# Kernel optimization log

Measured on AMD Instinct MI355X. Metric: run time of the kernel, lower is better.

The kernel has to match this reference:

```python
import jax, jax.numpy as jnp
import numpy as np

B = 1024; NOBJ = 8; NPAIRS = 28; NREL = 8; NNEG = NPAIRS - NREL
NFS = 2048; EFS = 1024; H1 = 128; H2 = 512

# upper-triangle pair ordering, identical to label_locating_matrix construction
_tri = np.array([(i, j) for i in range(NOBJ) for j in range(i + 1, NOBJ)], dtype=np.int64)
PAIR_I = jnp.asarray(_tri[:, 0])
PAIR_J = jnp.asarray(_tri[:, 1])
_llm = np.full((NOBJ, NOBJ), -1, dtype=np.int64)
for _p, (_i, _j) in enumerate(_tri):
    _llm[_i, _j] = _p
    _llm[_j, _i] = _p
LLM = jnp.asarray(_llm)


def setup_inputs() -> dict:
    key = jax.random.key(0)
    ks = jax.random.split(key, 12)
    # 8 distinct (i<j) object pairs per batch element
    rng = np.random.default_rng(0)
    locs = np.argsort(rng.random((B, NPAIRS)), axis=1)[:, :NREL]  # [B, 8] distinct pair slots
    object_pairs = jnp.asarray(_tri[locs])  # [B, 8, 2]
    s = 0.02
    return {
        "node_features": jax.random.normal(ks[0], (B, NOBJ, NFS), jnp.float32),
        "interaction_feature": jax.random.normal(ks[1], (B, NOBJ, NOBJ, EFS), jnp.float32),
        "object_pairs": object_pairs,
        "W_ind1": jax.random.normal(ks[2], (NFS + EFS, H1), jnp.float32) * s,
        "b_ind1": jnp.zeros((H1,), jnp.float32),
        "W_ind2": jax.random.normal(ks[3], (H1, 1), jnp.float32) * s,
        "b_ind2": jnp.zeros((1,), jnp.float32),
        "W_rel": jax.random.normal(ks[4], (NFS + EFS + H1, H2), jnp.float32) * s,
        "b_rel": jnp.zeros((H2,), jnp.float32),
        "W_cr": jax.random.normal(ks[5], (H2, 3), jnp.float32) * s,
        "b_cr": jnp.zeros((3,), jnp.float32),
        "W_lr": jax.random.normal(ks[6], (H2, 5), jnp.float32) * s,
        "b_lr": jnp.zeros((5,), jnp.float32),
        "W_mr": jax.random.normal(ks[7], (H2, 14), jnp.float32) * s,
        "b_mr": jnp.zeros((14,), jnp.float32),
    }


def reference(node_features, interaction_feature, object_pairs,
              W_ind1, b_ind1, W_ind2, b_ind2, W_rel, b_rel,
              W_cr, b_cr, W_lr, b_lr, W_mr, b_mr):
    # make_all_pairs (vectorized; num_obj == 8 so all 28 slots are filled)
    node_pair = 0.5 * (node_features[:, PAIR_I] + node_features[:, PAIR_J])  # [B,28,NFS]
    edge_pair = interaction_feature[:, PAIR_I, PAIR_J]                        # [B,28,EFS]
    feature_matrix = jnp.concatenate([node_pair, edge_pair], axis=-1)         # [B,28,NFS+EFS]

    pos_locs = LLM[object_pairs[..., 0], object_pairs[..., 1]]                # [B,8]
    b_idx = jnp.arange(B)[:, None]
    label_tensor = jnp.zeros((B, NPAIRS), jnp.float32).at[b_idx, pos_locs].set(1.0)

    # indeterminate branch (single Linear layers, no hidden ReLU)
    ind1 = feature_matrix @ W_ind1 + b_ind1                                   # [B,28,128]
    indeterminate_out = jax.nn.sigmoid(ind1 @ W_ind2 + b_ind2)[..., 0]        # [B,28]

    concat = jnp.concatenate([feature_matrix, ind1], axis=-1)                 # [B,28,NFS+EFS+128]
    rel = concat @ W_rel + b_rel                                              # [B,28,512]

    # separate_the_feats: gather positive slots, remaining slots (ascending) are negatives
    pos_features = jnp.take_along_axis(rel, pos_locs[..., None], axis=1)      # [B,8,512]
    neg_locs = jnp.argsort(label_tensor, axis=1, stable=True)[:, :NNEG]       # [B,20] ascending
    neg_features = jnp.take_along_axis(rel, neg_locs[..., None], axis=1)
    neg_features = neg_features.reshape(B * NNEG, H2)                          # [B*20,512]

    lr_pos = pos_features @ W_lr + b_lr
    cr_pos = pos_features @ W_cr + b_cr
    mr_pos = pos_features @ W_mr + b_mr
    lr_neg = neg_features @ W_lr + b_lr
    cr_neg = neg_features @ W_cr + b_cr
    mr_neg = neg_features @ W_mr + b_mr
    return (indeterminate_out, label_tensor, lr_pos, cr_pos, mr_pos, lr_neg, cr_neg, mr_neg)
```

## Files before the change

### kernel.cpp

```cpp
#include <hip/hip_runtime.h>
#include <hip/hip_bf16.h>
#include <cstdint>
#include <cstddef>

#define WS_BMAT 0
#define WS_BBIG 15360
#define WS_WBT  15424
#define WS_ND   64576
#define WS_ED   1571904

#define OUT_IND 0
#define OUT_LAB 28672
#define OUT_LRP 57344
#define OUT_CRP 98304
#define OUT_MRP 122880
#define OUT_LRN 237568
#define OUT_CRN 339968
#define OUT_MRN 401408

typedef __attribute__((ext_vector_type(8))) short bf16x8;
typedef __attribute__((ext_vector_type(4))) float f32x4;

__device__ __constant__ int d_pi[28] = {0,0,0,0,0,0,0,1,1,1,1,1,1,2,2,2,2,2,3,3,3,3,4,4,4,5,5,6};
__device__ __constant__ int d_pj[28] = {1,2,3,4,5,6,7,2,3,4,5,6,7,3,4,5,6,7,4,5,6,7,5,6,7,6,7,7};

__device__ __forceinline__ float wh_at(const float* wlr, const float* wcr, const float* wmr,
                                       int j, int h) {
  return (h < 5) ? wlr[j*5 + h] : (h < 8) ? wcr[j*3 + (h-5)] : wmr[j*14 + (h-8)];
}

__device__ __forceinline__ short f2bf(float f) {
  __hip_bfloat16 h = __float2bfloat16(f);
  short s;
  __builtin_memcpy(&s, &h, 2);
  return s;
}
__device__ __forceinline__ unsigned int f2bfu(float f) {
  __hip_bfloat16 h = __float2bfloat16(f);
  unsigned short s;
  __builtin_memcpy(&s, &h, 2);
  return (unsigned int)s;
}

__global__ __launch_bounds__(256) void prep1(
    const float* __restrict__ w_rel, const float* __restrict__ w_ind2,
    const float* __restrict__ w_lr, const float* __restrict__ w_cr, const float* __restrict__ w_mr,
    const float* __restrict__ b_ind1, const float* __restrict__ b_ind2,
    const float* __restrict__ b_rel,
    const float* __restrict__ b_lr, const float* __restrict__ b_cr, const float* __restrict__ b_mr,
    float* __restrict__ bmat, float* __restrict__ bbig) {
  int bid = blockIdx.x, tid = threadIdx.x;
  if (bid < 128) {
    int m = bid;
    __shared__ float swr[512];
    const float* wr2 = w_rel + (size_t)(3072 + m)*512;
    swr[tid]       = wr2[tid];
    swr[tid + 256] = wr2[tid + 256];
    __syncthreads();
    int h = tid >> 3, q = tid & 7;
    if (h < 22) {
      float a = 0.f;
#pragma unroll 8
      for (int jj = 0; jj < 64; ++jj) {
        int j = jj*8 + q;
        a = fmaf(swr[j], wh_at(w_lr, w_cr, w_mr, j, h), a);
      }
      a += __shfl_xor(a, 1); a += __shfl_xor(a, 2); a += __shfl_xor(a, 4);
      if (q == 0) bmat[(1 + h)*640 + m] = a;
    }
    if (tid == 248) bmat[0*640 + m]  = w_ind2[m];
    if (tid == 249) bmat[23*640 + m] = 0.f;
  } else if (bid == 128) {
    __shared__ float sbrel[512];
    for (int j = tid; j < 512; j += 256) {
      float a = b_rel[j];
#pragma unroll 4
      for (int m = 0; m < 128; ++m)
        a = fmaf(b_ind1[m], w_rel[(size_t)(3072 + m)*512 + j], a);
      sbrel[j] = a;
    }
    __syncthreads();
    int h = tid >> 3, q = tid & 7;
    if (h < 22) {
      float bh = (h < 5) ? b_lr[h] : (h < 8) ? b_cr[h-5] : b_mr[h-8];
      float a = 0.f;
#pragma unroll 8
      for (int jj = 0; jj < 64; ++jj) {
        int j = jj*8 + q;
        a = fmaf(sbrel[j], wh_at(w_lr, w_cr, w_mr, j, h), a);
      }
      a += __shfl_xor(a, 1); a += __shfl_xor(a, 2); a += __shfl_xor(a, 4);
      if (q == 0) bbig[1 + h] = a + bh;
    } else if (tid >= 248) {
      int q2 = tid & 7;
      float a = 0.f;
#pragma unroll
      for (int t = 0; t < 16; ++t)
        a = fmaf(b_ind1[q2*16 + t], w_ind2[q2*16 + t], a);
      a += __shfl_xor(a, 1); a += __shfl_xor(a, 2); a += __shfl_xor(a, 4);
      if (tid == 248) bbig[0]  = a + b_ind2[0];
      if (tid == 250) bbig[23] = 0.f;
    }
  } else {
    int idx = (bid - 129)*256 + tid;
    int j = idx / 24, n = idx % 24;
    float v = (n >= 1 && n <= 22) ? wh_at(w_lr, w_cr, w_mr, j, n - 1) : 0.f;
    bmat[n*640 + 128 + j] = v;
  }
}

__global__ __launch_bounds__(256) void prep2(
    const float* __restrict__ w_ind1, const float* __restrict__ w_rel,
    const float* __restrict__ bmat, unsigned int* __restrict__ wbT32) {
  int g = blockIdx.x*256 + threadIdx.x;
  int gid = g >> 2, q = g & 3;
  int kp = gid & 1, n = (gid >> 1) & 31, k2 = gid >> 6;
  int k = k2*2 + kp;
  float a = 0.f;
  if (n < 23) {
    const float* wr = w_rel + (size_t)k*512;
    const float* bn = bmat + n*640;
    if (q == 0) {
      const float* w1 = w_ind1 + (size_t)k*128;
#pragma unroll 8
      for (int i = 0; i < 128; ++i) a = fmaf(w1[i], bn[i], a);
#pragma unroll 8
      for (int j = 0; j < 32; ++j) a = fmaf(wr[j], bn[128 + j], a);
    } else {
      int j0 = 32 + (q - 1)*160;
#pragma unroll 8
      for (int jj = 0; jj < 160; ++jj) {
        int j = j0 + jj;
        a = fmaf(wr[j], bn[128 + j], a);
      }
    }
  }
  a += __shfl_xor(a, 1); a += __shfl_xor(a, 2);
  float other = __shfl_xor(a, 4);
  if (q == 0 && kp == 0) {
    unsigned int lo = f2bfu(a), hi = f2bfu(other);
    wbT32[(size_t)n*1536 + k2] = lo | (hi << 16);
  }
}

__global__ __launch_bounds__(256) void kmain_mfma(
    const float* __restrict__ nf, const float* __restrict__ intf,
    const unsigned short* __restrict__ wbT, float* __restrict__ ndp, float* __restrict__ edp) {
  __shared__ float red[4][1600];
  const int tid = threadIdx.x;
  const int l = tid & 63;
  const int w = tid >> 6;
  const int wid = blockIdx.x*4 + w;
  const bool isNode = wid < 1024;

  int rg, chunk, kbase;
  if (isNode) { rg = wid >> 3; chunk = wid & 7; kbase = 0; }
  else        { int e = wid - 1024; rg = e >> 2; chunk = e & 3; kbase = 2048; }
  const int R0 = rg*64;
  const int kd0 = chunk*256;

  const int ln = l & 15, lg = l >> 4;

  const float* xp[4];
#pragma unroll
  for (int i = 0; i < 4; ++i) {
    int grow = R0 + i*16 + ln;
    const float* rp;
    if (isNode) rp = nf + (size_t)grow*2048;
    else {
      int b = grow / 28, p = grow - b*28;
      rp = intf + (size_t)(b*64 + d_pi[p]*8 + d_pj[p])*1024;
    }
    xp[i] = rp + kd0 + lg*8;
  }
  const unsigned short* wp0 = wbT + (size_t)ln*3072 + kbase + kd0 + lg*8;
  const unsigned short* wp1 = wp0 + (size_t)16*3072;

  f32x4 acc[4][2];
#pragma unroll
  for (int i = 0; i < 4; ++i) {
    acc[i][0] = (f32x4){0.f, 0.f, 0.f, 0.f};
    acc[i][1] = (f32x4){0.f, 0.f, 0.f, 0.f};
  }

#pragma unroll 2
  for (int t = 0; t < 8; ++t) {
    const int ko = t*32;
    bf16x8 b0 = *(const bf16x8*)(wp0 + ko);
    bf16x8 b1 = *(const bf16x8*)(wp1 + ko);
#pragma unroll
    for (int i = 0; i < 4; ++i) {
      float4 xa = *(const float4*)(xp[i] + ko);
      float4 xb = *(const float4*)(xp[i] + ko + 4);
      bf16x8 a;
      a[0] = f2bf(xa.x); a[1] = f2bf(xa.y); a[2] = f2bf(xa.z); a[3] = f2bf(xa.w);
      a[4] = f2bf(xb.x); a[5] = f2bf(xb.y); a[6] = f2bf(xb.z); a[7] = f2bf(xb.w);
      acc[i][0] = __builtin_amdgcn_mfma_f32_16x16x32_bf16(a, b0, acc[i][0], 0, 0, 0);
      acc[i][1] = __builtin_amdgcn_mfma_f32_16x16x32_bf16(a, b1, acc[i][1], 0, 0, 0);
    }
  }

  float* rw = red[w];
#pragma unroll
  for (int i = 0; i < 4; ++i)
#pragma unroll
    for (int tn = 0; tn < 2; ++tn) {
      int n = tn*16 + ln;
      if (n < 23) {
#pragma unroll
        for (int r = 0; r < 4; ++r)
          rw[(i*16 + lg*4 + r)*25 + n] = acc[i][tn][r];
      }
    }
  __syncthreads();
  float* outp = isNode ? (ndp + ((size_t)chunk*8192  + R0)*23)
                       : (edp + ((size_t)chunk*28672 + R0)*23);
#pragma unroll
  for (int i = 0; i < 23; ++i) {
    int g = i*64 + l;
    int r = g / 23, n = g - r*23;
    outp[g] = rw[r*25 + n];
  }
}

__global__ __launch_bounds__(256) void kcombine(
    const float* __restrict__ ndp, const float* __restrict__ edp,
    const float* __restrict__ bbig, const int* __restrict__ opairs,
    float* __restrict__ out) {
  __shared__ float snd[184];
  __shared__ int spos[8];
  int b = blockIdx.x, tid = threadIdx.x;
  if (tid < 184) {
    int o = tid / 23, n = tid % 23;
    float s = 0.f;
#pragma unroll
    for (int c = 0; c < 8; ++c)
      s += ndp[((size_t)c*8192 + b*8 + o)*23 + n];
    snd[tid] = s;
  } else if (tid < 192) {
    int r = tid - 184;
    int oi = opairs[b*16 + r*2], oj = opairs[b*16 + r*2 + 1];
    int a = min(oi, oj), bb = max(oi, oj);
    spos[r] = 7*a - (a*(a+1))/2 + bb - 1;
  }
  __syncthreads();
  for (int g = tid; g < 644; g += 256) {
    int p = g / 23, n = g % 23;
    float ed = 0.f;
#pragma unroll
    for (int c = 0; c < 4; ++c)
      ed += edp[((size_t)c*28672 + b*28 + p)*23 + n];
    float val = 0.5f*(snd[d_pi[p]*23 + n] + snd[d_pj[p]*23 + n]) + ed + bbig[n];
    int slot = -1, below = 0;
#pragma unroll
    for (int r = 0; r < 8; ++r) {
      int pl = spos[r];
      slot = (pl == p) ? r : slot;
      below += (pl < p) ? 1 : 0;
    }
    if (n == 0) {
      out[OUT_IND + b*28 + p] = 1.f/(1.f + expf(-val));
      out[OUT_LAB + b*28 + p] = (slot >= 0) ? 1.f : 0.f;
    } else {
      int h = n - 1;
      if (slot >= 0) {
        int rr = b*8 + slot;
        if (h < 5)      out[OUT_LRP + rr*5  + h]     = val;
        else if (h < 8) out[OUT_CRP + rr*3  + (h-5)] = val;
        else            out[OUT_MRP + rr*14 + (h-8)] = val;
      } else {
        int s = p - below;
        int rr = b*20 + s;
        if (h < 5)      out[OUT_LRN + rr*5  + h]     = val;
        else if (h < 8) out[OUT_CRN + rr*3  + (h-5)] = val;
        else            out[OUT_MRN + rr*14 + (h-8)] = val;
      }
    }
  }
}

extern "C" void kernel_launch(void* const* d_in, const int* in_sizes, int n_in,
                              void* d_out, int out_size, void* d_ws, size_t ws_size,
                              hipStream_t stream) {
  const float* nf     = (const float*)d_in[0];
  const float* intf   = (const float*)d_in[1];
  const int*   opairs = (const int*)d_in[2];
  const float* w_ind1 = (const float*)d_in[3];
  const float* b_ind1 = (const float*)d_in[4];
  const float* w_ind2 = (const float*)d_in[5];
  const float* b_ind2 = (const float*)d_in[6];
  const float* w_rel  = (const float*)d_in[7];
  const float* b_rel  = (const float*)d_in[8];
  const float* w_cr   = (const float*)d_in[9];
  const float* b_cr   = (const float*)d_in[10];
  const float* w_lr   = (const float*)d_in[11];
  const float* b_lr   = (const float*)d_in[12];
  const float* w_mr   = (const float*)d_in[13];
  const float* b_mr   = (const float*)d_in[14];
  float* out = (float*)d_out;
  float* ws  = (float*)d_ws;

  float*          bmat  = ws + WS_BMAT;
  float*          bbig  = ws + WS_BBIG;
  unsigned int*   wbT32 = (unsigned int*)(ws + WS_WBT);
  unsigned short* wbT   = (unsigned short*)(ws + WS_WBT);
  float*          ndp   = ws + WS_ND;
  float*          edp   = ws + WS_ED;

  prep1<<<177, 256, 0, stream>>>(w_rel, w_ind2, w_lr, w_cr, w_mr,
                                 b_ind1, b_ind2, b_rel, b_lr, b_cr, b_mr, bmat, bbig);
  prep2<<<1536, 256, 0, stream>>>(w_ind1, w_rel, bmat, wbT32);
  kmain_mfma<<<704, 256, 0, stream>>>(nf, intf, wbT, ndp, edp);
  kcombine<<<1024, 256, 0, stream>>>(ndp, edp, bbig, opairs, out);
}
```

Measured before the change: 108.3 us.

## Stage activation tiles into LDS with double-buffered async global_load_lds

The main MFMA kernel now has each block handle 256 rows, 64 per wave. Activations are loaded through asynchronous global-to-LDS copies into a double buffer with an XOR swizzle, and the wait counters let the next K-step's load overlap the current step's MFMAs. The goal is to hide global memory latency, which previously stalled on direct register loads before each conversion and MFMA. In exchange the kernel uses 128 KB of LDS per block, which limits residency to about one block per CU, and it adds barriers between steps.

```diff
diff --git a/kernel.cpp b/kernel.cpp
--- a/kernel.cpp
+++ b/kernel.cpp
@@ -40,6 +40,11 @@
   unsigned short s;
   __builtin_memcpy(&s, &h, 2);
   return (unsigned int)s;
+}
+
+__device__ __forceinline__ void load_lds16(const float* g, float* l) {
+  __builtin_amdgcn_global_load_lds((const __attribute__((address_space(1))) void*)g,
+                                   (__attribute__((address_space(3))) void*)l, 16, 0, 0);
 }
 
 __global__ __launch_bounds__(256) void prep1(
@@ -143,36 +148,40 @@
   }
 }
 
-__global__ __launch_bounds__(256) void kmain_mfma(
+__global__ __launch_bounds__(256) void kmain_mfma2(
     const float* __restrict__ nf, const float* __restrict__ intf,
     const unsigned short* __restrict__ wbT, float* __restrict__ ndp, float* __restrict__ edp) {
-  __shared__ float red[4][1600];
+  __shared__ float smem[2][16384];
   const int tid = threadIdx.x;
   const int l = tid & 63;
   const int w = tid >> 6;
-  const int wid = blockIdx.x*4 + w;
-  const bool isNode = wid < 1024;
+  const int bid = blockIdx.x;
+  const bool isNode = bid < 256;
 
   int rg, chunk, kbase;
-  if (isNode) { rg = wid >> 3; chunk = wid & 7; kbase = 0; }
-  else        { int e = wid - 1024; rg = e >> 2; chunk = e & 3; kbase = 2048; }
-  const int R0 = rg*64;
+  if (isNode) { rg = bid >> 3; chunk = bid & 7; kbase = 0; }
+  else        { int e = bid - 256; rg = e >> 2; chunk = e & 3; kbase = 2048; }
+  const int R0 = rg*256;
   const int kd0 = chunk*256;
-
+  const int nsteps = 4;
+
+  const float* xsrc[16];
+  {
+    int sr = l >> 4, slot = l & 15;
+#pragma unroll
+    for (int i = 0; i < 16; ++i) {
+      int r = w*64 + i*4 + sr;
+      int grow = R0 + r;
+      const float* rp;
+      if (isNode) rp = nf + (size_t)grow*2048;
+      else {
+        int b = grow / 28, p = grow - b*28;
+        rp = intf + (size_t)(b*64 + d_pi[p]*8 + d_pj[p])*1024;
+      }
+      xsrc[i] = rp + kd0 + ((slot ^ (r & 7)) << 2);
+    }
+  }
   const int ln = l & 15, lg = l >> 4;
-
-  const float* xp[4];
-#pragma unroll
-  for (int i = 0; i < 4; ++i) {
-    int grow = R0 + i*16 + ln;
-    const float* rp;
-    if (isNode) rp = nf + (size_t)grow*2048;
-    else {
-      int b = grow / 28, p = grow - b*28;
-      rp = intf + (size_t)(b*64 + d_pi[p]*8 + d_pj[p])*1024;
-    }
-    xp[i] = rp + kd0 + lg*8;
-  }
   const unsigned short* wp0 = wbT + (size_t)ln*3072 + kbase + kd0 + lg*8;
   const unsigned short* wp1 = wp0 + (size_t)16*3072;
 
@@ -183,24 +192,50 @@
     acc[i][1] = (f32x4){0.f, 0.f, 0.f, 0.f};
   }
 
-#pragma unroll 2
-  for (int t = 0; t < 8; ++t) {
-    const int ko = t*32;
-    bf16x8 b0 = *(const bf16x8*)(wp0 + ko);
-    bf16x8 b1 = *(const bf16x8*)(wp1 + ko);
-#pragma unroll
-    for (int i = 0; i < 4; ++i) {
-      float4 xa = *(const float4*)(xp[i] + ko);
-      float4 xb = *(const float4*)(xp[i] + ko + 4);
-      bf16x8 a;
-      a[0] = f2bf(xa.x); a[1] = f2bf(xa.y); a[2] = f2bf(xa.z); a[3] = f2bf(xa.w);
-      a[4] = f2bf(xb.x); a[5] = f2bf(xb.y); a[6] = f2bf(xb.z); a[7] = f2bf(xb.w);
-      acc[i][0] = __builtin_amdgcn_mfma_f32_16x16x32_bf16(a, b0, acc[i][0], 0, 0, 0);
-      acc[i][1] = __builtin_amdgcn_mfma_f32_16x16x32_bf16(a, b1, acc[i][1], 0, 0, 0);
-    }
-  }
-
-  float* rw = red[w];
+#define STAGE(T, D) do {                                                        \
+    float* bd = &smem[D][0];                                                    \
+    _Pragma("unroll")                                                           \
+    for (int i = 0; i < 16; ++i)                                                \
+      load_lds16(xsrc[i] + (size_t)(T)*64, bd + (w*64 + i*4)*64);               \
+  } while (0)
+
+  STAGE(0, 0);
+
+#pragma unroll 1
+  for (int t = 0; t < nsteps; ++t) {
+    __builtin_amdgcn_s_barrier();
+    if (t + 1 < nsteps) {
+      STAGE(t + 1, (t + 1) & 1);
+      asm volatile("s_waitcnt vmcnt(16)" ::: "memory");
+    } else {
+      asm volatile("s_waitcnt vmcnt(0)" ::: "memory");
+    }
+
+    const float* bx = &smem[t & 1][0];
+#pragma unroll
+    for (int kt = 0; kt < 2; ++kt) {
+      const int koff = t*64 + kt*32;
+      bf16x8 b0 = *(const bf16x8*)(wp0 + koff);
+      bf16x8 b1 = *(const bf16x8*)(wp1 + koff);
+      const int q0 = kt*8 + lg*2;
+#pragma unroll
+      for (int i = 0; i < 4; ++i) {
+        int rloc = w*64 + i*16 + ln;
+        const float* rb = bx + rloc*64;
+        int sw = ln & 7;
+        float4 xa = *(const float4*)(rb + ((q0 ^ sw) << 2));
+        float4 xb = *(const float4*)(rb + (((q0 + 1) ^ sw) << 2));
+        bf16x8 a;
+        a[0] = f2bf(xa.x); a[1] = f2bf(xa.y); a[2] = f2bf(xa.z); a[3] = f2bf(xa.w);
+        a[4] = f2bf(xb.x); a[5] = f2bf(xb.y); a[6] = f2bf(xb.z); a[7] = f2bf(xb.w);
+        acc[i][0] = __builtin_amdgcn_mfma_f32_16x16x32_bf16(a, b0, acc[i][0], 0, 0, 0);
+        acc[i][1] = __builtin_amdgcn_mfma_f32_16x16x32_bf16(a, b1, acc[i][1], 0, 0, 0);
+      }
+    }
+  }
+#undef STAGE
+
+  float* rw = &smem[0][0] + w*4096;
 #pragma unroll
   for (int i = 0; i < 4; ++i)
 #pragma unroll
@@ -212,9 +247,8 @@
           rw[(i*16 + lg*4 + r)*25 + n] = acc[i][tn][r];
       }
     }
-  __syncthreads();
-  float* outp = isNode ? (ndp + ((size_t)chunk*8192  + R0)*23)
-                       : (edp + ((size_t)chunk*28672 + R0)*23);
+  float* outp = isNode ? (ndp + ((size_t)chunk*8192  + R0 + w*64)*23)
+                       : (edp + ((size_t)chunk*28672 + R0 + w*64)*23);
 #pragma unroll
   for (int i = 0; i < 23; ++i) {
     int g = i*64 + l;
@@ -310,6 +344,6 @@
   prep1<<<177, 256, 0, stream>>>(w_rel, w_ind2, w_lr, w_cr, w_mr,
                                  b_ind1, b_ind2, b_rel, b_lr, b_cr, b_mr, bmat, bbig);
   prep2<<<1536, 256, 0, stream>>>(w_ind1, w_rel, bmat, wbT32);
-  kmain_mfma<<<704, 256, 0, stream>>>(nf, intf, wbT, ndp, edp);
+  kmain_mfma2<<<704, 256, 0, stream>>>(nf, intf, wbT, ndp, edp);
   kcombine<<<1024, 256, 0, stream>>>(ndp, edp, bbig, opairs, out);
 }
```

New measurement: 119.4 us. 10.2% more time.
